# Kernel optimization log

Measured on AMD Instinct MI355X. Metric: run time of the kernel, lower is better.

## Reference

```python
import jax, jax.numpy as jnp
import numpy as np

N_TOKENS = 8192
D_MODEL = 1024
D_FF = 4096
N_EXPERTS = 8


def setup_inputs() -> dict:
    key = jax.random.key(0)
    ks = jax.random.split(key, 5)
    scale_in = 1.0 / np.sqrt(D_MODEL)
    x = jax.random.normal(ks[0], (N_TOKENS, D_MODEL), dtype=jnp.float32)
    gate_w = jax.random.normal(ks[1], (D_MODEL, N_EXPERTS), dtype=jnp.float32) * scale_in
    gate_b = jnp.zeros((N_EXPERTS,), dtype=jnp.float32)
    expert_w = jax.random.normal(ks[2], (N_EXPERTS, D_MODEL, D_FF), dtype=jnp.float32) * scale_in
    expert_b = jnp.zeros((N_EXPERTS, D_FF), dtype=jnp.float32)
    return {"x": x, "gate_w": gate_w, "gate_b": gate_b, "expert_w": expert_w, "expert_b": expert_b}


def reference(x, gate_w, gate_b, expert_w, expert_b):
    # Gate: [N, E] logits -> softmax -> top-1 expert per token
    gate_logits = x @ gate_w + gate_b
    gate_probs = jax.nn.softmax(gate_logits, axis=-1)
    top1 = jnp.argmax(gate_probs, axis=-1)  # [N], == argsort(...)[:, -1]

    # Dense all-expert compute, as in the original: [E, N, d_ff]
    expert_outputs = jnp.einsum('nd,edf->enf', x, expert_w) + expert_b[:, None, :]

    # Gather each token's top-1 expert output: [N, d_ff]
    selected = expert_outputs[top1, jnp.arange(x.shape[0])]
    return selected
```

## Files before the change

### kernel.cpp

```cpp
#include <hip/hip_runtime.h>


#define N_TOKENS 8192
#define D_MODEL  1024
#define D_FF     4096
#define N_EXPERTS 8

#define BM 128
#define BN 128
#define BK 32
#define MT_MAX (N_TOKENS / BM + N_EXPERTS)

typedef float  floatx4 __attribute__((ext_vector_type(4)));
typedef short  short8  __attribute__((ext_vector_type(8)));

__device__ __forceinline__ unsigned short f2bf(float f) {
    union { float f; unsigned u; } a; a.f = f;
    return (unsigned short)((a.u + 0x7fffu + ((a.u >> 16) & 1u)) >> 16);
}

#define GLDS(gp, lp) __builtin_amdgcn_global_load_lds( \
    (const __attribute__((address_space(1))) unsigned int*)(const void*)(gp), \
    (__attribute__((address_space(3))) unsigned int*)(void*)(lp), 16, 0, 0)

__global__ void init_counts(int* counts) {
    if (threadIdx.x < N_EXPERTS) counts[threadIdx.x] = 0;
}

__global__ __launch_bounds__(64) void gate_kernel(
    const float* __restrict__ x, const float* __restrict__ gw,
    const float* __restrict__ gb, unsigned short* __restrict__ xb,
    int* __restrict__ top1, int* __restrict__ counts)
{
    int n = blockIdx.x;
    int l = threadIdx.x;
    const float4* xr = (const float4*)(x + (size_t)n * D_MODEL);
    float acc[N_EXPERTS];
#pragma unroll
    for (int e = 0; e < N_EXPERTS; ++e) acc[e] = 0.f;

#pragma unroll
    for (int j = 0; j < 4; ++j) {
        int d4 = j * 64 + l;
        float4 v = xr[d4];
        float vv[4] = { v.x, v.y, v.z, v.w };
#pragma unroll
        for (int t = 0; t < 4; ++t) {
            const float4* g = (const float4*)(gw + (size_t)(d4 * 4 + t) * N_EXPERTS);
            float4 g0 = g[0], g1 = g[1];
            acc[0] += vv[t] * g0.x; acc[1] += vv[t] * g0.y;
            acc[2] += vv[t] * g0.z; acc[3] += vv[t] * g0.w;
            acc[4] += vv[t] * g1.x; acc[5] += vv[t] * g1.y;
            acc[6] += vv[t] * g1.z; acc[7] += vv[t] * g1.w;
        }
        union { unsigned short us[4]; uint2 u; } pk;
        pk.us[0] = f2bf(v.x); pk.us[1] = f2bf(v.y);
        pk.us[2] = f2bf(v.z); pk.us[3] = f2bf(v.w);
        ((uint2*)(xb + (size_t)n * D_MODEL))[d4] = pk.u;
    }
#pragma unroll
    for (int e = 0; e < N_EXPERTS; ++e)
        for (int off = 32; off > 0; off >>= 1)
            acc[e] += __shfl_down(acc[e], off);
    if (l == 0) {
        float best = acc[0] + gb[0]; int be = 0;
#pragma unroll
        for (int e = 1; e < N_EXPERTS; ++e) {
            float v = acc[e] + gb[e];
            if (v > best) { best = v; be = e; }
        }
        top1[n] = be;
        atomicAdd(&counts[be], 1);
    }
}

__global__ __launch_bounds__(256) void wconv_kernel(
    const float* __restrict__ w, unsigned short* __restrict__ wt)
{
    __shared__ unsigned short t[32][33];
    int e  = blockIdx.z;
    int f0 = blockIdx.x * 32;
    int d0 = blockIdx.y * 32;
    int tx = threadIdx.x, ty = threadIdx.y;
    const float* we = w + (size_t)e * D_MODEL * D_FF;
#pragma unroll
    for (int j = 0; j < 32; j += 8)
        t[ty + j][tx] = f2bf(we[(size_t)(d0 + ty + j) * D_FF + f0 + tx]);
    __syncthreads();
    unsigned short* wte = wt + (size_t)e * D_FF * D_MODEL;
#pragma unroll
    for (int j = 0; j < 32; j += 8)
        wte[(size_t)(f0 + ty + j) * D_MODEL + d0 + tx] = t[tx][ty + j];
}

__global__ void scan_kernel(const int* __restrict__ counts, int* __restrict__ poff,
                            int* __restrict__ tile_expert, int* __restrict__ list,
                            int* __restrict__ cursor)
{
    if (threadIdx.x == 0) {
        int off = 0;
        for (int e = 0; e < N_EXPERTS; ++e) {
            poff[e] = off;
            int nt = (counts[e] + BM - 1) / BM;
            for (int t = 0; t < nt; ++t) tile_expert[off / BM + t] = e;
            off += nt * BM;
        }
        for (int t = off / BM; t < MT_MAX; ++t) tile_expert[t] = -1;
    }
    if (threadIdx.x < N_EXPERTS) cursor[threadIdx.x] = 0;
    for (int i = threadIdx.x; i < MT_MAX * BM; i += blockDim.x) list[i] = -1;
}

__global__ void scatter_kernel(const int* __restrict__ top1, const int* __restrict__ poff,
                               int* __restrict__ cursor, int* __restrict__ list)
{
    int n = blockIdx.x * 256 + threadIdx.x;
    if (n < N_TOKENS) {
        int e = top1[n];
        int slot = atomicAdd(&cursor[e], 1);
        list[poff[e] + slot] = n;
    }
}

__global__ __launch_bounds__(256) void gemm_kernel(
    const unsigned short* __restrict__ xb,
    const unsigned short* __restrict__ wt,
    const float* __restrict__ eb,
    const int* __restrict__ tile_expert,
    const int* __restrict__ list,
    float* __restrict__ out)
{
    int e = tile_expert[blockIdx.x];
    if (e < 0) return;
    int n0 = blockIdx.y * BN;

    __shared__ unsigned short As[BM * BK];
    __shared__ unsigned short Bs[BN * BK];
    __shared__ int toks[BM];

    int tid = threadIdx.x;
    int lane = tid & 63, wave = tid >> 6;
    if (tid < BM) toks[tid] = list[blockIdx.x * BM + tid];
    __syncthreads();

    int c0 = (wave * 2 + 0) * 64 + lane;
    int c1 = (wave * 2 + 1) * 64 + lane;
    int ar0 = c0 >> 2, ac0 = (c0 & 3) * 8;
    int ar1 = c1 >> 2, ac1 = (c1 & 3) * 8;
    int ta0 = toks[ar0]; if (ta0 < 0) ta0 = 0;
    int ta1 = toks[ar1]; if (ta1 < 0) ta1 = 0;
    const unsigned short* gA0 = xb + (size_t)ta0 * D_MODEL + ac0;
    const unsigned short* gA1 = xb + (size_t)ta1 * D_MODEL + ac1;
    const unsigned short* wbase = wt + (size_t)e * D_FF * D_MODEL;
    const unsigned short* gB0 = wbase + (size_t)(n0 + ar0) * D_MODEL + ac0;
    const unsigned short* gB1 = wbase + (size_t)(n0 + ar1) * D_MODEL + ac1;
    unsigned short* lA0 = As + (wave * 2 + 0) * 512;
    unsigned short* lA1 = As + (wave * 2 + 1) * 512;
    unsigned short* lB0 = Bs + (wave * 2 + 0) * 512;
    unsigned short* lB1 = Bs + (wave * 2 + 1) * 512;

    floatx4 acc[4][4];
#pragma unroll
    for (int mi = 0; mi < 4; ++mi)
#pragma unroll
        for (int ni = 0; ni < 4; ++ni)
            acc[mi][ni] = (floatx4){0.f, 0.f, 0.f, 0.f};

    int mw = (wave >> 1) * 64;
    int nw = (wave & 1) * 64;
    int q = lane >> 4, r = lane & 15;

    for (int k0 = 0; k0 < D_MODEL; k0 += BK) {
        GLDS(gA0 + k0, lA0);
        GLDS(gA1 + k0, lA1);
        GLDS(gB0 + k0, lB0);
        GLDS(gB1 + k0, lB1);
        __syncthreads();

        short8 af[4], bf[4];
#pragma unroll
        for (int mi = 0; mi < 4; ++mi)
            af[mi] = *(const short8*)&As[(mw + mi * 16 + r) * BK + q * 8];
#pragma unroll
        for (int ni = 0; ni < 4; ++ni)
            bf[ni] = *(const short8*)&Bs[(nw + ni * 16 + r) * BK + q * 8];
#pragma unroll
        for (int mi = 0; mi < 4; ++mi)
#pragma unroll
            for (int ni = 0; ni < 4; ++ni)
                acc[mi][ni] = __builtin_amdgcn_mfma_f32_16x16x32_bf16(
                    af[mi], bf[ni], acc[mi][ni], 0, 0, 0);
        __syncthreads();
    }

#pragma unroll
    for (int ni = 0; ni < 4; ++ni) {
        int f = n0 + nw + ni * 16 + r;
        float bias = eb[(size_t)e * D_FF + f];
#pragma unroll
        for (int mi = 0; mi < 4; ++mi) {
            int mbase = mw + mi * 16 + q * 4;
#pragma unroll
            for (int i = 0; i < 4; ++i) {
                int tok = toks[mbase + i];
                if (tok >= 0) out[(size_t)tok * D_FF + f] = acc[mi][ni][i] + bias;
            }
        }
    }
}

extern "C" void kernel_launch(void* const* d_in, const int* in_sizes, int n_in,
                              void* d_out, int out_size, void* d_ws, size_t ws_size,
                              hipStream_t stream) {
    const float* x  = (const float*)d_in[0];
    const float* gw = (const float*)d_in[1];
    const float* gb = (const float*)d_in[2];
    const float* ew = (const float*)d_in[3];
    const float* eb = (const float*)d_in[4];
    float* out = (float*)d_out;

    char* ws = (char*)d_ws;
    int* top1        = (int*)ws;
    int* counts      = (int*)(ws + 32768);
    int* cursor      = (int*)(ws + 32768 + 64);
    int* poff        = (int*)(ws + 32768 + 128);
    int* tile_expert = (int*)(ws + 32768 + 256);
    int* list        = (int*)(ws + 36864);
    unsigned short* xb = (unsigned short*)(ws + 131072);
    unsigned short* wt = (unsigned short*)(ws + 131072 + (size_t)N_TOKENS * D_MODEL * 2);

    hipLaunchKernelGGL(init_counts, dim3(1), dim3(64), 0, stream, counts);
    hipLaunchKernelGGL(gate_kernel, dim3(N_TOKENS), dim3(64), 0, stream,
                       x, gw, gb, xb, top1, counts);
    hipLaunchKernelGGL(wconv_kernel, dim3(D_FF / 32, D_MODEL / 32, N_EXPERTS), dim3(32, 8),
                       0, stream, ew, wt);
    hipLaunchKernelGGL(scan_kernel, dim3(1), dim3(256), 0, stream,
                       counts, poff, tile_expert, list, cursor);
    hipLaunchKernelGGL(scatter_kernel, dim3(N_TOKENS / 256), dim3(256), 0, stream,
                       top1, poff, cursor, list);
    hipLaunchKernelGGL(gemm_kernel, dim3(MT_MAX, D_FF / BN), dim3(256), 0, stream,
                       xb, wt, eb, tile_expert, list, out);
}
```

Baseline: 516.2 us.

## Double-buffer GEMM LDS, remap tiles per XCD, vectorize weight conversion and scatter

The grouped GEMM now double-buffers the A and B tiles in LDS, prefetching the next K slice while the current one is computed, and drops the second barrier per iteration. Blocks are remapped onto a 1D grid so that the N-tiles of one M-tile spread across the 8 XCDs, which is meant to improve L2 reuse of the expert weights. The weight transpose-and-convert kernel switches to 64x64 tiles with float4 loads and 16-byte stores. The scatter uses wave-aggregated atomics, and the gate kernel packs 4 tokens per block. The GEMM doubles its LDS use, which may reduce occupancy.

After: 504.4 us. -2.3%, faster.

```diff
diff --git a/kernel.cpp b/kernel.cpp
--- a/kernel.cpp
+++ b/kernel.cpp
@@ -9,7 +9,9 @@
 #define BM 128
 #define BN 128
 #define BK 32
+#define NKT (D_MODEL / BK)
 #define MT_MAX (N_TOKENS / BM + N_EXPERTS)
+#define NTILES (D_FF / BN)
 
 typedef float  floatx4 __attribute__((ext_vector_type(4)));
 typedef short  short8  __attribute__((ext_vector_type(8)));
@@ -27,13 +29,14 @@
     if (threadIdx.x < N_EXPERTS) counts[threadIdx.x] = 0;
 }
 
-__global__ __launch_bounds__(64) void gate_kernel(
+__global__ __launch_bounds__(256) void gate_kernel(
     const float* __restrict__ x, const float* __restrict__ gw,
     const float* __restrict__ gb, unsigned short* __restrict__ xb,
     int* __restrict__ top1, int* __restrict__ counts)
 {
-    int n = blockIdx.x;
-    int l = threadIdx.x;
+    int wave = threadIdx.x >> 6;
+    int l    = threadIdx.x & 63;
+    int n = blockIdx.x * 4 + wave;
     const float4* xr = (const float4*)(x + (size_t)n * D_MODEL);
     float acc[N_EXPERTS];
 #pragma unroll
@@ -74,23 +77,46 @@
     }
 }
 
+#define WST 68
 __global__ __launch_bounds__(256) void wconv_kernel(
     const float* __restrict__ w, unsigned short* __restrict__ wt)
 {
-    __shared__ unsigned short t[32][33];
+    __shared__ unsigned short tt[64 * WST];
     int e  = blockIdx.z;
-    int f0 = blockIdx.x * 32;
-    int d0 = blockIdx.y * 32;
-    int tx = threadIdx.x, ty = threadIdx.y;
-    const float* we = w + (size_t)e * D_MODEL * D_FF;
-#pragma unroll
-    for (int j = 0; j < 32; j += 8)
-        t[ty + j][tx] = f2bf(we[(size_t)(d0 + ty + j) * D_FF + f0 + tx]);
+    int f0 = blockIdx.x * 64;
+    int d0 = blockIdx.y * 64;
+    int t  = threadIdx.x;
+    const float* we = w + (size_t)e * D_MODEL * D_FF + (size_t)d0 * D_FF + f0;
+
+    int fg = (t & 15) * 4;
+    int dg = (t >> 4) * 4;
+    unsigned short v[4][4];
+#pragma unroll
+    for (int j = 0; j < 4; ++j) {
+        float4 r = *(const float4*)(we + (size_t)(dg + j) * D_FF + fg);
+        v[0][j] = f2bf(r.x); v[1][j] = f2bf(r.y);
+        v[2][j] = f2bf(r.z); v[3][j] = f2bf(r.w);
+    }
+#pragma unroll
+    for (int i = 0; i < 4; ++i) {
+        union { unsigned short us[4]; uint2 u; } pk;
+        pk.us[0] = v[i][0]; pk.us[1] = v[i][1];
+        pk.us[2] = v[i][2]; pk.us[3] = v[i][3];
+        *(uint2*)&tt[(fg + i) * WST + dg] = pk.u;
+    }
     __syncthreads();
-    unsigned short* wte = wt + (size_t)e * D_FF * D_MODEL;
-#pragma unroll
-    for (int j = 0; j < 32; j += 8)
-        wte[(size_t)(f0 + ty + j) * D_MODEL + d0 + tx] = t[tx][ty + j];
+
+    unsigned short* wte = wt + (size_t)e * D_FF * D_MODEL + (size_t)f0 * D_MODEL + d0;
+    int fr = t >> 3;
+    int dr = (t & 7) * 8;
+#pragma unroll
+    for (int p = 0; p < 2; ++p) {
+        int f = fr + p * 32;
+        uint2 a = *(const uint2*)&tt[f * WST + dr];
+        uint2 b = *(const uint2*)&tt[f * WST + dr + 4];
+        uint4 o; o.x = a.x; o.y = a.y; o.z = b.x; o.w = b.y;
+        *(uint4*)(wte + (size_t)f * D_MODEL + dr) = o;
+    }
 }
 
 __global__ void scan_kernel(const int* __restrict__ counts, int* __restrict__ poff,
@@ -111,15 +137,26 @@
     for (int i = threadIdx.x; i < MT_MAX * BM; i += blockDim.x) list[i] = -1;
 }
 
-__global__ void scatter_kernel(const int* __restrict__ top1, const int* __restrict__ poff,
-                               int* __restrict__ cursor, int* __restrict__ list)
+__global__ __launch_bounds__(256) void scatter_kernel(
+    const int* __restrict__ top1, const int* __restrict__ poff,
+    int* __restrict__ cursor, int* __restrict__ list)
 {
     int n = blockIdx.x * 256 + threadIdx.x;
-    if (n < N_TOKENS) {
-        int e = top1[n];
-        int slot = atomicAdd(&cursor[e], 1);
-        list[poff[e] + slot] = n;
-    }
+    int l = threadIdx.x & 63;
+    int e = top1[n];
+    int slot = 0;
+#pragma unroll
+    for (int e0 = 0; e0 < N_EXPERTS; ++e0) {
+        unsigned long long m = __ballot(e == e0);
+        if (e == e0) {
+            int leader = __ffsll((unsigned long long)m) - 1;
+            int base = 0;
+            if (l == leader) base = atomicAdd(&cursor[e0], __popcll(m));
+            base = __shfl(base, leader);
+            slot = base + __popcll(m & ((1ull << l) - 1ull));
+        }
+    }
+    list[poff[e] + slot] = n;
 }
 
 __global__ __launch_bounds__(256) void gemm_kernel(
@@ -130,17 +167,21 @@
     const int* __restrict__ list,
     float* __restrict__ out)
 {
-    int e = tile_expert[blockIdx.x];
+    int bid = blockIdx.x;
+    int xcd = bid & 7, w = bid >> 3;
+    int mt  = w >> 2;
+    int nt  = (xcd << 2) | (w & 3);
+    int e = tile_expert[mt];
     if (e < 0) return;
-    int n0 = blockIdx.y * BN;
-
-    __shared__ unsigned short As[BM * BK];
-    __shared__ unsigned short Bs[BN * BK];
+    int n0 = nt * BN;
+
+    __shared__ unsigned short As[2][BM * BK];
+    __shared__ unsigned short Bs[2][BN * BK];
     __shared__ int toks[BM];
 
     int tid = threadIdx.x;
     int lane = tid & 63, wave = tid >> 6;
-    if (tid < BM) toks[tid] = list[blockIdx.x * BM + tid];
+    if (tid < BM) toks[tid] = list[mt * BM + tid];
     __syncthreads();
 
     int c0 = (wave * 2 + 0) * 64 + lane;
@@ -154,10 +195,8 @@
     const unsigned short* wbase = wt + (size_t)e * D_FF * D_MODEL;
     const unsigned short* gB0 = wbase + (size_t)(n0 + ar0) * D_MODEL + ac0;
     const unsigned short* gB1 = wbase + (size_t)(n0 + ar1) * D_MODEL + ac1;
-    unsigned short* lA0 = As + (wave * 2 + 0) * 512;
-    unsigned short* lA1 = As + (wave * 2 + 1) * 512;
-    unsigned short* lB0 = Bs + (wave * 2 + 0) * 512;
-    unsigned short* lB1 = Bs + (wave * 2 + 1) * 512;
+    int o0 = (wave * 2 + 0) * 512;
+    int o1 = (wave * 2 + 1) * 512;
 
     floatx4 acc[4][4];
 #pragma unroll
@@ -170,27 +209,34 @@
     int nw = (wave & 1) * 64;
     int q = lane >> 4, r = lane & 15;
 
-    for (int k0 = 0; k0 < D_MODEL; k0 += BK) {
-        GLDS(gA0 + k0, lA0);
-        GLDS(gA1 + k0, lA1);
-        GLDS(gB0 + k0, lB0);
-        GLDS(gB1 + k0, lB1);
+    GLDS(gA0, &As[0][o0]);
+    GLDS(gA1, &As[0][o1]);
+    GLDS(gB0, &Bs[0][o0]);
+    GLDS(gB1, &Bs[0][o1]);
+
+    for (int kt = 0; kt < NKT; ++kt) {
+        int cur = kt & 1;
         __syncthreads();
-
+        if (kt + 1 < NKT) {
+            int k1 = (kt + 1) * BK;
+            GLDS(gA0 + k1, &As[cur ^ 1][o0]);
+            GLDS(gA1 + k1, &As[cur ^ 1][o1]);
+            GLDS(gB0 + k1, &Bs[cur ^ 1][o0]);
+            GLDS(gB1 + k1, &Bs[cur ^ 1][o1]);
+        }
         short8 af[4], bf[4];
 #pragma unroll
         for (int mi = 0; mi < 4; ++mi)
-            af[mi] = *(const short8*)&As[(mw + mi * 16 + r) * BK + q * 8];
+            af[mi] = *(const short8*)&As[cur][(mw + mi * 16 + r) * BK + q * 8];
 #pragma unroll
         for (int ni = 0; ni < 4; ++ni)
-            bf[ni] = *(const short8*)&Bs[(nw + ni * 16 + r) * BK + q * 8];
+            bf[ni] = *(const short8*)&Bs[cur][(nw + ni * 16 + r) * BK + q * 8];
 #pragma unroll
         for (int mi = 0; mi < 4; ++mi)
 #pragma unroll
             for (int ni = 0; ni < 4; ++ni)
                 acc[mi][ni] = __builtin_amdgcn_mfma_f32_16x16x32_bf16(
                     af[mi], bf[ni], acc[mi][ni], 0, 0, 0);
-        __syncthreads();
     }
 
 #pragma unroll
@@ -230,14 +276,14 @@
     unsigned short* wt = (unsigned short*)(ws + 131072 + (size_t)N_TOKENS * D_MODEL * 2);
 
     hipLaunchKernelGGL(init_counts, dim3(1), dim3(64), 0, stream, counts);
-    hipLaunchKernelGGL(gate_kernel, dim3(N_TOKENS), dim3(64), 0, stream,
+    hipLaunchKernelGGL(gate_kernel, dim3(N_TOKENS / 4), dim3(256), 0, stream,
                        x, gw, gb, xb, top1, counts);
-    hipLaunchKernelGGL(wconv_kernel, dim3(D_FF / 32, D_MODEL / 32, N_EXPERTS), dim3(32, 8),
+    hipLaunchKernelGGL(wconv_kernel, dim3(D_FF / 64, D_MODEL / 64, N_EXPERTS), dim3(256),
                        0, stream, ew, wt);
     hipLaunchKernelGGL(scan_kernel, dim3(1), dim3(256), 0, stream,
                        counts, poff, tile_expert, list, cursor);
     hipLaunchKernelGGL(scatter_kernel, dim3(N_TOKENS / 256), dim3(256), 0, stream,
                        top1, poff, cursor, list);
-    hipLaunchKernelGGL(gemm_kernel, dim3(MT_MAX, D_FF / BN), dim3(256), 0, stream,
+    hipLaunchKernelGGL(gemm_kernel, dim3(MT_MAX * NTILES), dim3(256), 0, stream,
                        xb, wt, eb, tile_expert, list, out);
 }
```
